# Kernel tuning notes

Measured on AMD Instinct MI355X. Metric: run time of the kernel, lower is better.

The kernel has to match this reference:

```python
import jax, jax.numpy as jnp
import numpy as np

H, B, S, E, V, C = 1024, 1024, 128, 6, 3, 10


def setup_inputs() -> dict:
    key = jax.random.key(0)
    ks = jax.random.split(key, 18)
    sH = 1.0 / np.sqrt(H)

    def n(k, shape, scale):
        return (jax.random.normal(k, shape, dtype=jnp.float32) * scale)

    return {
        'x': jax.random.randint(ks[0], (B, S), 0, V),
        'emb': n(ks[1], (V, E), 1.0),
        'W_gx': n(ks[2], (H, E), 1.0 / np.sqrt(E)),
        'W_gh': n(ks[3], (H, H), sH),
        'b_g': n(ks[4], (H, 1), sH),
        'W_ix': n(ks[5], (H, E), 1.0 / np.sqrt(E)),
        'W_ih': n(ks[6], (H, H), sH),
        'b_i': n(ks[7], (H, 1), sH),
        'W_fx': n(ks[8], (H, E), 1.0 / np.sqrt(E)),
        'W_fh': n(ks[9], (H, H), sH),
        'b_f': n(ks[10], (H, 1), sH),
        'W_ox': n(ks[11], (H, E), 1.0 / np.sqrt(E)),
        'W_oh': n(ks[12], (H, H), sH),
        'b_o': n(ks[13], (H, 1), sH),
        'W_ph': n(ks[14], (C, H), sH),
        'b_p': n(ks[15], (C, 1), sH),
        'h_init': n(ks[16], (H, B), 1.0),
        'c_init': n(ks[17], (H, B), 1.0),
    }


def reference(x, emb, W_gx, W_gh, b_g, W_ix, W_ih, b_i, W_fx, W_fh, b_f,
              W_ox, W_oh, b_o, W_ph, b_p, h_init, c_init):
    T = x.shape[1] - 1  # torch loop runs over seq_length - 1 steps
    e = emb[x[:, :T]]  # [B, T, E]
    # Precompute all input-to-gate projections in one batched contraction each.
    Xg = jnp.einsum('he,bte->thb', W_gx, e)  # [T, H, B]
    Xi = jnp.einsum('he,bte->thb', W_ix, e)
    Xf = jnp.einsum('he,bte->thb', W_fx, e)
    Xo = jnp.einsum('he,bte->thb', W_ox, e)

    def step(carry, xs):
        h, c = carry  # [H, B]
        xg, xi, xf, xo = xs
        g = jnp.tanh(xg + W_gh @ h + b_g)
        i = jax.nn.sigmoid(xi + W_ih @ h + b_i)
        f = jax.nn.sigmoid(xf + W_fh @ h + b_f)
        o = jax.nn.sigmoid(xo + W_oh @ h + b_o)
        c2 = g * i + c * f
        h2 = jnp.tanh(c2) * o
        return (h2, c2), None

    (h, c), _ = jax.lax.scan(step, (h_init, c_init), (Xg, Xi, Xf, Xo))
    p = W_ph @ h + b_p  # [C, B]
    return jax.nn.log_softmax(p.T, axis=-1)  # [B, C]
```

## Files before the change

kernel.cpp:

```cpp
#include <hip/hip_runtime.h>

constexpr int kH = 1024;
constexpr int kB = 1024;
constexpr int kS = 128;
constexpr int kT = 127;
constexpr int kE = 6;
constexpr int kV = 3;
constexpr int kC = 10;

typedef short s16x8 __attribute__((ext_vector_type(8)));
typedef short s16x4 __attribute__((ext_vector_type(4)));
typedef float f32x4 __attribute__((ext_vector_type(4)));
typedef unsigned short u16;

__device__ __forceinline__ float b2f(u16 u) {
    return __uint_as_float(((unsigned)u) << 16);
}
__device__ __forceinline__ u16 f2b(float f) {
    unsigned u = __float_as_uint(f);
    return (u16)((u + 0x7FFFu + ((u >> 16) & 1u)) >> 16);
}
__device__ __forceinline__ float sigmoid_fast(float x) {
    return 1.0f / (1.0f + __expf(-x));
}
__device__ __forceinline__ float tanh_fast(float x) {
    return 2.0f / (1.0f + __expf(-2.0f * x)) - 1.0f;
}
__device__ __forceinline__ float clamp30(float x) {
    return fminf(fmaxf(x, -30.0f), 30.0f);
}

__device__ __forceinline__ void async_copy16(const u16* g, u16* l) {
    __builtin_amdgcn_global_load_lds(
        (const __attribute__((address_space(1))) void*)g,
        (__attribute__((address_space(3))) void*)l, 16, 0, 0);
}

__global__ __launch_bounds__(256) void prep_weights(
    const float* __restrict__ Wgh, const float* __restrict__ Wih,
    const float* __restrict__ Wfh, const float* __restrict__ Woh,
    u16* __restrict__ wsw)
{
    unsigned grp = blockIdx.x * 256 + threadIdx.x;
    const int lane = grp & 63;
    const int lm   = lane & 15;
    const int quad = lane >> 4;
    const int k0   = (grp >> 6) & 7;
    const int g    = (grp >> 9) & 3;
    const int kc   = (grp >> 11) & 3;
    const int by   = grp >> 13;
    const float* src = (g == 0) ? Wgh : (g == 1) ? Wih : (g == 2) ? Wfh : Woh;
    const int row = by * 16 + lm;
    const int k   = kc * 256 + k0 * 32 + quad * 8;
    f32x4 v0 = *(const f32x4*)(src + (size_t)row * kH + k);
    f32x4 v1 = *(const f32x4*)(src + (size_t)row * kH + k + 4);
    s16x8 o;
#pragma unroll
    for (int j = 0; j < 4; ++j) o[j] = (short)f2b(v0[j]);
#pragma unroll
    for (int j = 0; j < 4; ++j) o[4 + j] = (short)f2b(v1[j]);
    *(s16x8*)(wsw + (size_t)grp * 8) = o;
}

__global__ __launch_bounds__(1024) void prep_hc(
    const float* __restrict__ h0, const float* __restrict__ c0,
    u16* __restrict__ hA, float* __restrict__ cT)
{
    __shared__ float th[32][33];
    __shared__ float tc[32][33];
    int b = blockIdx.x * 32 + threadIdx.x;
    int h = blockIdx.y * 32 + threadIdx.y;
    th[threadIdx.y][threadIdx.x] = h0[(size_t)h * kB + b];
    tc[threadIdx.y][threadIdx.x] = c0[(size_t)h * kB + b];
    __syncthreads();
    int ob = blockIdx.x * 32 + threadIdx.y;
    int oh = blockIdx.y * 32 + threadIdx.x;
    hA[(size_t)ob * kH + oh] = f2b(th[threadIdx.x][threadIdx.y]);
    cT[(size_t)ob * kH + oh] = tc[threadIdx.x][threadIdx.y];
}

__global__ __launch_bounds__(256) void prep_q(
    const float* __restrict__ Wgx, const float* __restrict__ Wix,
    const float* __restrict__ Wfx, const float* __restrict__ Wox,
    const float* __restrict__ bg,  const float* __restrict__ bi,
    const float* __restrict__ bf_, const float* __restrict__ bo,
    const float* __restrict__ emb, float* __restrict__ Qp)
{
    int tid = blockIdx.x * blockDim.x + threadIdx.x;
    if (tid >= 4096) return;
    int g   = tid >> 10;
    int hr4 = (tid & 1023) >> 2;
    int v   = tid & 3;
    const float* Wx = (g == 0) ? Wgx : (g == 1) ? Wix : (g == 2) ? Wfx : Wox;
    const float* bb = (g == 0) ? bg  : (g == 1) ? bi  : (g == 2) ? bf_ : bo;
    f32x4 o;
#pragma unroll
    for (int reg = 0; reg < 4; ++reg) {
        int row = hr4 * 4 + reg;
        float s = bb[row];
        if (v < kV) {
#pragma unroll
            for (int e = 0; e < kE; ++e) s += Wx[row * kE + e] * emb[v * kE + e];
        }
        o[reg] = s;
    }
    *(f32x4*)(Qp + (size_t)tid * 4) = o;
}

__global__ __launch_bounds__(256, 2) void lstm_step(
    const u16* __restrict__ wsw, const float* __restrict__ Qp,
    const int* __restrict__ x, int t,
    const short* __restrict__ hin, u16* __restrict__ hout,
    float* __restrict__ cT)
{
    __shared__ u16 wlds[2][16384];

    const int tid  = threadIdx.x;
    const int lane = tid & 63;
    const int wave = tid >> 6;
    const int lm   = lane & 15;
    const int quad = lane >> 4;
    const int blk  = blockIdx.x;
    const int xcd  = blk & 7;
    const int slot = blk >> 3;
    const int by   = xcd * 8 + (slot & 7);
    const int bx   = slot >> 3;
    const int r0 = by * 16;
    const int c0 = bx * 128 + wave * 32;

    const u16* wswblk = wsw + (size_t)by * 65536;

#pragma unroll
    for (int rr = 0; rr < 8; ++rr) {
        const int ub = wave * 4096 + rr * 512;
        async_copy16(wswblk + ub + lane * 8, &wlds[0][ub]);
    }

    int vv[2];
#pragma unroll
    for (int nt = 0; nt < 2; ++nt) {
        int v = x[(size_t)(c0 + nt * 16 + lm) * kS + t];
        vv[nt] = (v < 0) ? 0 : (v > kV - 1) ? (kV - 1) : v;
    }
    f32x4 qv[2][4];
#pragma unroll
    for (int nt = 0; nt < 2; ++nt)
#pragma unroll
        for (int g = 0; g < 4; ++g)
            qv[nt][g] = *(const f32x4*)(Qp +
                (size_t)(((g * 256 + by * 4 + quad) * 4 + vv[nt]) * 4));
    f32x4 cold[2];
#pragma unroll
    for (int nt = 0; nt < 2; ++nt)
        cold[nt] = *(const f32x4*)(cT +
            (size_t)(c0 + nt * 16 + lm) * kH + r0 + quad * 4);

    const int koff = quad * 8;
    const short* hrow0 = hin + (size_t)(c0 + lm) * kH + koff;
    const short* hrow1 = hin + (size_t)(c0 + 16 + lm) * kH + koff;
    s16x8 br[6][2];
#pragma unroll
    for (int s = 0; s < 5; ++s) {
        br[s][0] = *(const s16x8*)(hrow0 + s * 32);
        br[s][1] = *(const s16x8*)(hrow1 + s * 32);
    }

    f32x4 acc[4][2];
    const f32x4 zero = {0.f, 0.f, 0.f, 0.f};
#pragma unroll
    for (int g = 0; g < 4; ++g)
#pragma unroll
        for (int n = 0; n < 2; ++n) acc[g][n] = zero;

    asm volatile("s_waitcnt vmcnt(0)" ::: "memory");
    __syncthreads();

#pragma unroll
    for (int k0 = 0; k0 < 32; ++k0) {
        if ((k0 & 7) == 0 && k0 > 0) {
            asm volatile("s_waitcnt vmcnt(0)" ::: "memory");
            __syncthreads();
        }
        if ((k0 & 7) == 0 && k0 < 24) {
            const int nc = (k0 >> 3) + 1;
            const u16* gsrc = wswblk + (size_t)nc * 16384;
#pragma unroll
            for (int rr = 0; rr < 8; ++rr) {
                const int ub = wave * 4096 + rr * 512;
                async_copy16(gsrc + ub + lane * 8, &wlds[nc & 1][ub]);
            }
        }
        if (k0 + 5 < 32) {
            const int s = (k0 + 5) % 6;
            br[s][0] = *(const s16x8*)(hrow0 + (k0 + 5) * 32);
            br[s][1] = *(const s16x8*)(hrow1 + (k0 + 5) * 32);
        }
        const int cur = k0 % 6;
        const int buf = (k0 >> 3) & 1;
#pragma unroll
        for (int g = 0; g < 4; ++g) {
            const int f = ((g * 8 + (k0 & 7)) * 64 + lane) * 8;
            s16x8 a = *(const s16x8*)&wlds[buf][f];
            acc[g][0] = __builtin_amdgcn_mfma_f32_16x16x32_bf16(a, br[cur][0], acc[g][0], 0, 0, 0);
            acc[g][1] = __builtin_amdgcn_mfma_f32_16x16x32_bf16(a, br[cur][1], acc[g][1], 0, 0, 0);
        }
    }

#pragma unroll
    for (int nt = 0; nt < 2; ++nt) {
        const int c = c0 + nt * 16 + lm;
        const int rb = r0 + quad * 4;
        f32x4 cnew;
        s16x4 hnew;
#pragma unroll
        for (int reg = 0; reg < 4; ++reg) {
            float pg = clamp30(acc[0][nt][reg] + qv[nt][0][reg]);
            float pi = clamp30(acc[1][nt][reg] + qv[nt][1][reg]);
            float pf = clamp30(acc[2][nt][reg] + qv[nt][2][reg]);
            float po = clamp30(acc[3][nt][reg] + qv[nt][3][reg]);
            float gg = tanh_fast(pg);
            float ii = sigmoid_fast(pi);
            float ff = sigmoid_fast(pf);
            float oo = sigmoid_fast(po);
            float c2 = gg * ii + cold[nt][reg] * ff;
            c2 = fminf(fmaxf(c2, -200.0f), 200.0f);
            cnew[reg] = c2;
            hnew[reg] = (short)f2b(tanh_fast(c2) * oo);
        }
        *(f32x4*)(cT + (size_t)c * kH + rb) = cnew;
        *(s16x4*)(hout + (size_t)c * kH + rb) = hnew;
    }
}

__global__ __launch_bounds__(256) void logits_kernel(
    const u16* __restrict__ hT, const float* __restrict__ Wph,
    const float* __restrict__ bp, float* __restrict__ out)
{
    const int wave = threadIdx.x >> 6;
    const int lane = threadIdx.x & 63;
    const int b = blockIdx.x * 4 + wave;

    const u16* hp = hT + (size_t)b * kH + lane * 16;
    float hf[16];
#pragma unroll
    for (int j = 0; j < 16; ++j) hf[j] = b2f(hp[j]);

    float p[kC];
#pragma unroll
    for (int cls = 0; cls < kC; ++cls) {
        const float* wp = Wph + (size_t)cls * kH + lane * 16;
        float s = 0.f;
#pragma unroll
        for (int j = 0; j < 16; ++j) s += hf[j] * wp[j];
#pragma unroll
        for (int off = 1; off < 64; off <<= 1) s += __shfl_xor(s, off, 64);
        p[cls] = fminf(fmaxf(s + bp[cls], -1.0e4f), 1.0e4f);
    }

    float m = p[0];
#pragma unroll
    for (int cls = 1; cls < kC; ++cls) m = fmaxf(m, p[cls]);
    float se = 0.f;
#pragma unroll
    for (int cls = 0; cls < kC; ++cls) se += __expf(p[cls] - m);
    float l = m + __logf(se);

    if (lane < kC) {
        float myp = p[0];
#pragma unroll
        for (int cls = 1; cls < kC; ++cls)
            if (lane == cls) myp = p[cls];
        out[(size_t)b * kC + lane] = myp - l;
    }
}

extern "C" void kernel_launch(void* const* d_in, const int* in_sizes, int n_in,
                              void* d_out, int out_size, void* d_ws, size_t ws_size,
                              hipStream_t stream)
{
    const int*   x   = (const int*)  d_in[0];
    const float* emb = (const float*)d_in[1];
    const float* Wgx = (const float*)d_in[2];
    const float* Wgh = (const float*)d_in[3];
    const float* bg  = (const float*)d_in[4];
    const float* Wix = (const float*)d_in[5];
    const float* Wih = (const float*)d_in[6];
    const float* bi  = (const float*)d_in[7];
    const float* Wfx = (const float*)d_in[8];
    const float* Wfh = (const float*)d_in[9];
    const float* bf_ = (const float*)d_in[10];
    const float* Wox = (const float*)d_in[11];
    const float* Woh = (const float*)d_in[12];
    const float* bo  = (const float*)d_in[13];
    const float* Wph = (const float*)d_in[14];
    const float* bp  = (const float*)d_in[15];
    const float* h0  = (const float*)d_in[16];
    const float* c0  = (const float*)d_in[17];

    char* ws = (char*)d_ws;
    float* Qp  = (float*)ws;
    u16*   hA  = (u16*)(ws + (64 << 10));
    u16*   hB  = hA + (size_t)kB * kH;
    float* cT  = (float*)(hB + (size_t)kB * kH);
    u16*   wsw = (u16*)(cT + (size_t)kB * kH);

    prep_weights<<<dim3(2048), dim3(256), 0, stream>>>(Wgh, Wih, Wfh, Woh, wsw);
    prep_hc<<<dim3(kB / 32, kH / 32), dim3(32, 32), 0, stream>>>(h0, c0, hA, cT);
    prep_q<<<dim3(16), dim3(256), 0, stream>>>(Wgx, Wix, Wfx, Wox, bg, bi, bf_, bo, emb, Qp);

    for (int t = 0; t < kT; ++t) {
        const u16* hin  = (t & 1) ? hB : hA;
        u16*       hout = (t & 1) ? hA : hB;
        lstm_step<<<dim3(512), dim3(256), 0, stream>>>(
            wsw, Qp, x, t, (const short*)hin, hout, cT);
    }
    logits_kernel<<<dim3(kB / 4), dim3(256), 0, stream>>>(hB, Wph, bp, (float*)d_out);
}
```

Before: 2.937 ms.

## Fuse all LSTM timesteps into one persistent kernel with flag-based grid barrier

The 127 per-timestep kernel launches are replaced by a single persistent kernel. It loops over time, keeps the cell state in registers and synchronises all 512 blocks through per-block flag counters polled in global memory. This removes launch overhead and the cT read/write traffic each step. In exchange it depends on all 512 blocks being co-resident (2 per CU under the launch bounds), or the spin barrier deadlocks, and the cross-block polling adds barrier latency. The weights are still reloaded from global into LDS every step.

```diff
diff --git a/kernel.cpp b/kernel.cpp
--- a/kernel.cpp
+++ b/kernel.cpp
@@ -11,6 +11,8 @@
 typedef short s16x8 __attribute__((ext_vector_type(8)));
 typedef short s16x4 __attribute__((ext_vector_type(4)));
 typedef float f32x4 __attribute__((ext_vector_type(4)));
+typedef int   i32x2 __attribute__((ext_vector_type(2)));
+typedef int   i32x4 __attribute__((ext_vector_type(4)));
 typedef unsigned short u16;
 
 __device__ __forceinline__ float b2f(u16 u) {
@@ -84,9 +86,11 @@
     const float* __restrict__ Wfx, const float* __restrict__ Wox,
     const float* __restrict__ bg,  const float* __restrict__ bi,
     const float* __restrict__ bf_, const float* __restrict__ bo,
-    const float* __restrict__ emb, float* __restrict__ Qp)
+    const float* __restrict__ emb, float* __restrict__ Qp,
+    int* __restrict__ flags)
 {
     int tid = blockIdx.x * blockDim.x + threadIdx.x;
+    if (tid < 512) flags[tid] = 0;
     if (tid >= 4096) return;
     int g   = tid >> 10;
     int hr4 = (tid & 1023) >> 2;
@@ -107,11 +111,11 @@
     *(f32x4*)(Qp + (size_t)tid * 4) = o;
 }
 
-__global__ __launch_bounds__(256, 2) void lstm_step(
+__global__ __launch_bounds__(256, 2) void lstm_persist(
     const u16* __restrict__ wsw, const float* __restrict__ Qp,
-    const int* __restrict__ x, int t,
-    const short* __restrict__ hin, u16* __restrict__ hout,
-    float* __restrict__ cT)
+    const int* __restrict__ x,
+    short* __restrict__ hA, short* __restrict__ hB,
+    const float* __restrict__ cT, int* __restrict__ flags)
 {
     __shared__ u16 wlds[2][16384];
 
@@ -130,105 +134,147 @@
 
     const u16* wswblk = wsw + (size_t)by * 65536;
 
-#pragma unroll
-    for (int rr = 0; rr < 8; ++rr) {
-        const int ub = wave * 4096 + rr * 512;
-        async_copy16(wswblk + ub + lane * 8, &wlds[0][ub]);
-    }
-
-    int vv[2];
-#pragma unroll
-    for (int nt = 0; nt < 2; ++nt) {
-        int v = x[(size_t)(c0 + nt * 16 + lm) * kS + t];
-        vv[nt] = (v < 0) ? 0 : (v > kV - 1) ? (kV - 1) : v;
-    }
-    f32x4 qv[2][4];
+    f32x4 creg[2];
 #pragma unroll
     for (int nt = 0; nt < 2; ++nt)
+        creg[nt] = *(const f32x4*)(cT +
+            (size_t)(c0 + nt * 16 + lm) * kH + r0 + quad * 4);
+
+    const int* xp0 = x + (size_t)(c0 + lm) * kS;
+    const int* xp1 = x + (size_t)(c0 + 16 + lm) * kS;
+    const int koff = quad * 8;
+
+#pragma unroll 1
+    for (int t = 0; t < kT; ++t) {
+        const short* hin  = (t & 1) ? hB : hA;
+        short*       hout = (t & 1) ? hA : hB;
+
+#pragma unroll
+        for (int rr = 0; rr < 8; ++rr) {
+            const int ub = wave * 4096 + rr * 512;
+            async_copy16(wswblk + ub + lane * 8, &wlds[0][ub]);
+        }
+
+        int vv[2];
+        {
+            int v0 = xp0[t]; vv[0] = (v0 < 0) ? 0 : (v0 > kV - 1) ? (kV - 1) : v0;
+            int v1 = xp1[t]; vv[1] = (v1 < 0) ? 0 : (v1 > kV - 1) ? (kV - 1) : v1;
+        }
+        f32x4 qv[2][4];
+#pragma unroll
+        for (int nt = 0; nt < 2; ++nt)
+#pragma unroll
+            for (int g = 0; g < 4; ++g)
+                qv[nt][g] = *(const f32x4*)(Qp +
+                    (size_t)(((g * 256 + by * 4 + quad) * 4 + vv[nt]) * 4));
+
+        const short* hrow0 = hin + (size_t)(c0 + lm) * kH + koff;
+        const short* hrow1 = hin + (size_t)(c0 + 16 + lm) * kH + koff;
+        s16x8 br[6][2];
+#pragma unroll
+        for (int s = 0; s < 5; ++s) {
+            br[s][0] = *(const s16x8*)(hrow0 + s * 32);
+            br[s][1] = *(const s16x8*)(hrow1 + s * 32);
+        }
+
+        f32x4 acc[4][2];
+        const f32x4 zero = {0.f, 0.f, 0.f, 0.f};
 #pragma unroll
         for (int g = 0; g < 4; ++g)
-            qv[nt][g] = *(const f32x4*)(Qp +
-                (size_t)(((g * 256 + by * 4 + quad) * 4 + vv[nt]) * 4));
-    f32x4 cold[2];
-#pragma unroll
-    for (int nt = 0; nt < 2; ++nt)
-        cold[nt] = *(const f32x4*)(cT +
-            (size_t)(c0 + nt * 16 + lm) * kH + r0 + quad * 4);
-
-    const int koff = quad * 8;
-    const short* hrow0 = hin + (size_t)(c0 + lm) * kH + koff;
-    const short* hrow1 = hin + (size_t)(c0 + 16 + lm) * kH + koff;
-    s16x8 br[6][2];
-#pragma unroll
-    for (int s = 0; s < 5; ++s) {
-        br[s][0] = *(const s16x8*)(hrow0 + s * 32);
-        br[s][1] = *(const s16x8*)(hrow1 + s * 32);
-    }
-
-    f32x4 acc[4][2];
-    const f32x4 zero = {0.f, 0.f, 0.f, 0.f};
-#pragma unroll
-    for (int g = 0; g < 4; ++g)
-#pragma unroll
-        for (int n = 0; n < 2; ++n) acc[g][n] = zero;
-
-    asm volatile("s_waitcnt vmcnt(0)" ::: "memory");
-    __syncthreads();
-
-#pragma unroll
-    for (int k0 = 0; k0 < 32; ++k0) {
-        if ((k0 & 7) == 0 && k0 > 0) {
+#pragma unroll
+            for (int n = 0; n < 2; ++n) acc[g][n] = zero;
+
+        asm volatile("s_waitcnt vmcnt(0)" ::: "memory");
+        __syncthreads();
+
+#pragma unroll
+        for (int k0 = 0; k0 < 32; ++k0) {
+            if ((k0 & 7) == 0 && k0 > 0) {
+                asm volatile("s_waitcnt vmcnt(0)" ::: "memory");
+                __syncthreads();
+            }
+            if ((k0 & 7) == 0 && k0 < 24) {
+                const int nc = (k0 >> 3) + 1;
+                const u16* gsrc = wswblk + (size_t)nc * 16384;
+#pragma unroll
+                for (int rr = 0; rr < 8; ++rr) {
+                    const int ub = wave * 4096 + rr * 512;
+                    async_copy16(gsrc + ub + lane * 8, &wlds[nc & 1][ub]);
+                }
+            }
+            if (k0 + 5 < 32) {
+                const int s = (k0 + 5) % 6;
+                br[s][0] = *(const s16x8*)(hrow0 + (k0 + 5) * 32);
+                br[s][1] = *(const s16x8*)(hrow1 + (k0 + 5) * 32);
+            }
+            const int cur = k0 % 6;
+            const int buf = (k0 >> 3) & 1;
+#pragma unroll
+            for (int g = 0; g < 4; ++g) {
+                const int f = ((g * 8 + (k0 & 7)) * 64 + lane) * 8;
+                s16x8 a = *(const s16x8*)&wlds[buf][f];
+                acc[g][0] = __builtin_amdgcn_mfma_f32_16x16x32_bf16(a, br[cur][0], acc[g][0], 0, 0, 0);
+                acc[g][1] = __builtin_amdgcn_mfma_f32_16x16x32_bf16(a, br[cur][1], acc[g][1], 0, 0, 0);
+            }
+        }
+
+#pragma unroll
+        for (int nt = 0; nt < 2; ++nt) {
+            const int c = c0 + nt * 16 + lm;
+            const int rb = r0 + quad * 4;
+            f32x4 cnew;
+            s16x4 hnew;
+#pragma unroll
+            for (int reg = 0; reg < 4; ++reg) {
+                float pg = clamp30(acc[0][nt][reg] + qv[nt][0][reg]);
+                float pi = clamp30(acc[1][nt][reg] + qv[nt][1][reg]);
+                float pf = clamp30(acc[2][nt][reg] + qv[nt][2][reg]);
+                float po = clamp30(acc[3][nt][reg] + qv[nt][3][reg]);
+                float gg = tanh_fast(pg);
+                float ii = sigmoid_fast(pi);
+                float ff = sigmoid_fast(pf);
+                float oo = sigmoid_fast(po);
+                float c2 = gg * ii + creg[nt][reg] * ff;
+                c2 = fminf(fmaxf(c2, -200.0f), 200.0f);
+                cnew[reg] = c2;
+                hnew[reg] = (short)f2b(tanh_fast(c2) * oo);
+            }
+            creg[nt] = cnew;
+            i32x2 hv;
+            __builtin_memcpy(&hv, &hnew, 8);
+            short* hp = hout + (size_t)c * kH + rb;
+            asm volatile("global_store_dwordx2 %0, %1, off sc0 sc1"
+                         :: "v"(hp), "v"(hv) : "memory");
+        }
+
+        if (t < kT - 1) {
             asm volatile("s_waitcnt vmcnt(0)" ::: "memory");
             __syncthreads();
-        }
-        if ((k0 & 7) == 0 && k0 < 24) {
-            const int nc = (k0 >> 3) + 1;
-            const u16* gsrc = wswblk + (size_t)nc * 16384;
-#pragma unroll
-            for (int rr = 0; rr < 8; ++rr) {
-                const int ub = wave * 4096 + rr * 512;
-                async_copy16(gsrc + ub + lane * 8, &wlds[nc & 1][ub]);
-            }
-        }
-        if (k0 + 5 < 32) {
-            const int s = (k0 + 5) % 6;
-            br[s][0] = *(const s16x8*)(hrow0 + (k0 + 5) * 32);
-            br[s][1] = *(const s16x8*)(hrow1 + (k0 + 5) * 32);
-        }
-        const int cur = k0 % 6;
-        const int buf = (k0 >> 3) & 1;
-#pragma unroll
-        for (int g = 0; g < 4; ++g) {
-            const int f = ((g * 8 + (k0 & 7)) * 64 + lane) * 8;
-            s16x8 a = *(const s16x8*)&wlds[buf][f];
-            acc[g][0] = __builtin_amdgcn_mfma_f32_16x16x32_bf16(a, br[cur][0], acc[g][0], 0, 0, 0);
-            acc[g][1] = __builtin_amdgcn_mfma_f32_16x16x32_bf16(a, br[cur][1], acc[g][1], 0, 0, 0);
-        }
-    }
-
-#pragma unroll
-    for (int nt = 0; nt < 2; ++nt) {
-        const int c = c0 + nt * 16 + lm;
-        const int rb = r0 + quad * 4;
-        f32x4 cnew;
-        s16x4 hnew;
-#pragma unroll
-        for (int reg = 0; reg < 4; ++reg) {
-            float pg = clamp30(acc[0][nt][reg] + qv[nt][0][reg]);
-            float pi = clamp30(acc[1][nt][reg] + qv[nt][1][reg]);
-            float pf = clamp30(acc[2][nt][reg] + qv[nt][2][reg]);
-            float po = clamp30(acc[3][nt][reg] + qv[nt][3][reg]);
-            float gg = tanh_fast(pg);
-            float ii = sigmoid_fast(pi);
-            float ff = sigmoid_fast(pf);
-            float oo = sigmoid_fast(po);
-            float c2 = gg * ii + cold[nt][reg] * ff;
-            c2 = fminf(fmaxf(c2, -200.0f), 200.0f);
-            cnew[reg] = c2;
-            hnew[reg] = (short)f2b(tanh_fast(c2) * oo);
-        }
-        *(f32x4*)(cT + (size_t)c * kH + rb) = cnew;
-        *(s16x4*)(hout + (size_t)c * kH + rb) = hnew;
+            if (tid < 64) {
+                if (tid == 0) {
+                    int* fp = flags + blk;
+                    int fv = t + 1;
+                    asm volatile("global_store_dword %0, %1, off sc0 sc1\n\t"
+                                 "s_waitcnt vmcnt(0)"
+                                 :: "v"(fp), "v"(fv) : "memory");
+                }
+                const int* fp = flags + lane * 8;
+                for (;;) {
+                    i32x4 fa, fb;
+                    asm volatile(
+                        "global_load_dwordx4 %0, %2, off sc0 sc1\n\t"
+                        "global_load_dwordx4 %1, %2, off offset:16 sc0 sc1\n\t"
+                        "s_waitcnt vmcnt(0)"
+                        : "=&v"(fa), "=&v"(fb) : "v"(fp) : "memory");
+                    int ok = (fa.x > t) & (fa.y > t) & (fa.z > t) & (fa.w > t) &
+                             (fb.x > t) & (fb.y > t) & (fb.z > t) & (fb.w > t);
+                    if (__all(ok)) break;
+                    __builtin_amdgcn_s_sleep(1);
+                }
+                __builtin_amdgcn_fence(__ATOMIC_ACQUIRE, "agent");
+            }
+            __syncthreads();
+        }
     }
 }
 
@@ -303,16 +349,15 @@
     u16*   hB  = hA + (size_t)kB * kH;
     float* cT  = (float*)(hB + (size_t)kB * kH);
     u16*   wsw = (u16*)(cT + (size_t)kB * kH);
+    int*   flags = (int*)(wsw + (size_t)64 * 65536);
 
     prep_weights<<<dim3(2048), dim3(256), 0, stream>>>(Wgh, Wih, Wfh, Woh, wsw);
     prep_hc<<<dim3(kB / 32, kH / 32), dim3(32, 32), 0, stream>>>(h0, c0, hA, cT);
-    prep_q<<<dim3(16), dim3(256), 0, stream>>>(Wgx, Wix, Wfx, Wox, bg, bi, bf_, bo, emb, Qp);
-
-    for (int t = 0; t < kT; ++t) {
-        const u16* hin  = (t & 1) ? hB : hA;
-        u16*       hout = (t & 1) ? hA : hB;
-        lstm_step<<<dim3(512), dim3(256), 0, stream>>>(
-            wsw, Qp, x, t, (const short*)hin, hout, cT);
-    }
+    prep_q<<<dim3(16), dim3(256), 0, stream>>>(Wgx, Wix, Wfx, Wox, bg, bi, bf_, bo,
+                                               emb, Qp, flags);
+
+    lstm_persist<<<dim3(512), dim3(256), 0, stream>>>(
+        wsw, Qp, x, (short*)hA, (short*)hB, cT, flags);
+
     logits_kernel<<<dim3(kB / 4), dim3(256), 0, stream>>>(hB, Wph, bp, (float*)d_out);
 }
```

New measurement: 3.710 ms. 26.3% more time.
